# Performance work log

Measured on AMD Instinct MI355X. Metric: run time of the kernel, lower is better.

Reference implementation:

```python
import jax, jax.numpy as jnp
import numpy as np

T, B, IN, H, L = 300, 32, 320, 1024, 3  # seq, batch, input, hidden, layers (bidirectional)


def _init_params(key):
    stdv = 1.0 / np.sqrt(H)
    ks = jax.random.split(key, 8)
    u = lambda k, shp: jax.random.uniform(k, shp, jnp.float32, -stdv, stdv)
    # layer 0 (input IN), 2 directions
    w_ih0 = u(ks[0], (2, 4 * H, IN))
    w_hh0 = u(ks[1], (2, 4 * H, H))
    b_ih0 = u(ks[2], (2, 4 * H))
    b_hh0 = u(ks[3], (2, 4 * H))
    # layers 1..L-1 (input 2H), 2 directions
    w_ihL = u(ks[4], (L - 1, 2, 4 * H, 2 * H))
    w_hhL = u(ks[5], (L - 1, 2, 4 * H, H))
    b_ihL = u(ks[6], (L - 1, 2, 4 * H))
    b_hhL = u(ks[7], (L - 1, 2, 4 * H))
    # forget_gate_bias = 1.0 applied to bias_ih[H:2H], bias_hh[H:2H] = 0
    fgb = 1.0
    b_ih0 = b_ih0.at[:, H:2 * H].set(fgb)
    b_hh0 = b_hh0.at[:, H:2 * H].set(0.0)
    b_ihL = b_ihL.at[:, :, H:2 * H].set(fgb)
    b_hhL = b_hhL.at[:, :, H:2 * H].set(0.0)
    return dict(w_ih0=w_ih0, w_hh0=w_hh0, b_ih0=b_ih0, b_hh0=b_hh0,
                w_ihL=w_ihL, w_hhL=w_hhL, b_ihL=b_ihL, b_hhL=b_hhL)


def setup_inputs() -> dict:
    key = jax.random.key(0)
    k1, k2 = jax.random.split(key)
    inp = {
        "x": jax.random.normal(k1, (T, B, IN), jnp.float32),
        "h0": jnp.zeros((L * 2, B, H), jnp.float32),
        "c0": jnp.zeros((L * 2, B, H), jnp.float32),
    }
    inp.update(_init_params(k2))
    return inp


def _hard_sigmoid(z):
    return jnp.clip(0.2 * z + 0.5, 0.0, 1.0)


def _lstm_dir(x_seq, w_ih, w_hh, b_ih, b_hh, h0, c0, reverse):
    # x_seq: [T, B, D_in]; returns ys [T,B,H], (h,c) [B,H]
    xs = jnp.flip(x_seq, 0) if reverse else x_seq
    gx = jnp.einsum('tbi,gi->tbg', xs, w_ih) + b_ih + b_hh  # [T,B,4H]

    def step(carry, gxt):
        h, c = carry
        gates = gxt + h @ w_hh.T
        i, f, g, o = jnp.split(gates, 4, axis=-1)
        i = _hard_sigmoid(i)
        f = _hard_sigmoid(f)
        g = jnp.clip(g, -1.0, 1.0)  # hardtanh
        o = _hard_sigmoid(o)
        c = f * c + i * g
        h = o * jnp.clip(c, -1.0, 1.0)
        return (h, c), h

    (h, c), ys = jax.lax.scan(step, (h0, c0), gx)
    if reverse:
        ys = jnp.flip(ys, 0)
    return ys, h, c


def _stacked_forward(x, h0, c0, w_ih0, w_hh0, b_ih0, b_hh0, w_ihL, w_hhL, b_ihL, b_hhL):
    # Faithful to StackedLSTM: hn = hx[0].view(L,2,B,H); cn = hn (source bug: cell
    # init comes from h0, c0 ignored). h0/c0 are zeros so this is also correct math.
    hn = h0.reshape(L, 2, B, H)
    cn = hn
    out = x
    hs, cs = [], []
    for l in range(L):
        if l == 0:
            wih, whh, bih, bhh = w_ih0, w_hh0, b_ih0, b_hh0
        else:
            wih, whh, bih, bhh = w_ihL[l - 1], w_hhL[l - 1], b_ihL[l - 1], b_hhL[l - 1]
        yf, hf, cf = _lstm_dir(out, wih[0], whh[0], bih[0], bhh[0], hn[l, 0], cn[l, 0], False)
        yb, hb, cb = _lstm_dir(out, wih[1], whh[1], bih[1], bhh[1], hn[l, 1], cn[l, 1], True)
        out = jnp.concatenate([yf, yb], axis=-1)  # [T,B,2H]
        hs += [hf, hb]
        cs += [cf, cb]
    hn_out = jnp.stack(hs)  # [L*2, B, H]
    cn_out = jnp.stack(cs)
    return out, hn_out, cn_out


def reference(x, h0, c0, w_ih0, w_hh0, b_ih0, b_hh0, w_ihL, w_hhL, b_ihL, b_hhL):
    return _stacked_forward(x, h0, c0, w_ih0, w_hh0, b_ih0, b_hh0,
                            w_ihL, w_hhL, b_ihL, b_hhL)
```

## Files before the change

### kernel.cpp

```cpp
#include <hip/hip_runtime.h>

typedef __bf16 bf16;
typedef __attribute__((ext_vector_type(8))) __bf16 bf16x8;
typedef __attribute__((ext_vector_type(4))) float f32x4;

#define GLOBAL_AS __attribute__((address_space(1)))
#define LDS_AS __attribute__((address_space(3)))

__device__ __forceinline__ void gload_lds16(const void* g, void* l) {
  __builtin_amdgcn_global_load_lds((const GLOBAL_AS void*)g, (LDS_AS void*)l, 16, 0, 0);
}
__device__ __forceinline__ void gload_lds16_cc(const void* g, void* l) {
  __builtin_amdgcn_global_load_lds((const GLOBAL_AS void*)g, (LDS_AS void*)l, 16, 0, 0x11);
}

__device__ __forceinline__ f32x4 mfma16(bf16x8 a, bf16x8 b, f32x4 c) {
  return __builtin_amdgcn_mfma_f32_16x16x32_bf16(a, b, c, 0, 0, 0);
}

#define GBAR() asm volatile("s_barrier" ::: "memory")

#define T_SEQ 300
#define NBATCH 32
#define DIN 320
#define NH 1024
#define NG 4096
#define MROWS 9600
#define OUT_Y 19660800
#define HN_SZ 196608
#define FPAD 32

__global__ __launch_bounds__(256) void k_cvt(const float* __restrict__ src,
                                             bf16* __restrict__ dst, int n8) {
  int stride = gridDim.x * blockDim.x;
  for (int i = blockIdx.x * blockDim.x + threadIdx.x; i < n8; i += stride) {
    const float* s = src + (size_t)i * 8;
    f32x4 a = *(const f32x4*)s;
    f32x4 b = *(const f32x4*)(s + 4);
    bf16x8 o;
#pragma unroll
    for (int j = 0; j < 4; ++j) { o[j] = (bf16)a[j]; o[j + 4] = (bf16)b[j]; }
    *(bf16x8*)(dst + (size_t)i * 8) = o;
  }
}

__global__ __launch_bounds__(256) void k_bsum(const float* __restrict__ bih0,
                                              const float* __restrict__ bhh0,
                                              const float* __restrict__ bihL,
                                              const float* __restrict__ bhhL,
                                              float* __restrict__ bsum) {
  int i = blockIdx.x * 256 + threadIdx.x;
  if (i < 2 * NG) bsum[i] = bih0[i] + bhh0[i];
  else            bsum[i] = bihL[i - 2 * NG] + bhhL[i - 2 * NG];
}

__global__ __launch_bounds__(256) void k_gemm_gx(const bf16* __restrict__ A,
                                                 const bf16* __restrict__ Bw,
                                                 const float* __restrict__ bias,
                                                 bf16* __restrict__ gxout, int K) {
  __shared__ bf16 As[128 * 32];
  __shared__ bf16 Bs[128 * 32];
  const int t = threadIdx.x;
  const int m0 = blockIdx.y * 128, n0 = blockIdx.x * 128;
  const int lane = t & 63, wid = t >> 6;
  const int wr = wid >> 1, wc = wid & 1;
  const int fr = lane & 15, fq = lane >> 4;
  f32x4 acc[4][4] = {};
  for (int k0 = 0; k0 < K; k0 += 32) {
#pragma unroll
    for (int r = 0; r < 2; ++r) {
      int idx = r * 256 + t;
      int row = idx >> 2, kk = (idx & 3) * 8;
      gload_lds16(A + (size_t)(m0 + row) * K + k0 + kk, As + (size_t)idx * 8);
      gload_lds16(Bw + (size_t)(n0 + row) * K + k0 + kk, Bs + (size_t)idx * 8);
    }
    asm volatile("s_waitcnt vmcnt(0)" ::: "memory");
    __syncthreads();
    bf16x8 af[4], bf_[4];
#pragma unroll
    for (int i2 = 0; i2 < 4; ++i2) {
      af[i2]  = *(const bf16x8*)(As + (wr * 64 + i2 * 16 + fr) * 32 + fq * 8);
      bf_[i2] = *(const bf16x8*)(Bs + (wc * 64 + i2 * 16 + fr) * 32 + fq * 8);
    }
#pragma unroll
    for (int mi = 0; mi < 4; ++mi)
#pragma unroll
      for (int ni = 0; ni < 4; ++ni)
        acc[mi][ni] = mfma16(af[mi], bf_[ni], acc[mi][ni]);
    __syncthreads();
  }
#pragma unroll
  for (int ni = 0; ni < 4; ++ni) {
    int col = n0 + wc * 64 + ni * 16 + fr;
    float bv = bias[col];
    int dir = col >> 12, grow = col & (NG - 1);
    int gg = grow >> 10, uu = grow & 1023;
    bf16* base = gxout + ((size_t)dir * 300 * 4 + gg) * 32768 + uu;
#pragma unroll
    for (int mi = 0; mi < 4; ++mi) {
#pragma unroll
      for (int j = 0; j < 4; ++j) {
        int row = m0 + wr * 64 + mi * 16 + fq * 4 + j;
        int tt = row >> 5, b = row & 31;
        base[(size_t)tt * 131072 + b * 1024] = (bf16)(acc[mi][ni][j] + bv);
      }
    }
  }
}

__global__ __launch_bounds__(256) void k_init(const float* __restrict__ h0,
                                              bf16* __restrict__ hbuf,
                                              int* __restrict__ flags, int layer) {
  int i = blockIdx.x * 256 + threadIdx.x;
  hbuf[i] = (bf16)h0[(size_t)layer * 65536 + i];
  if (blockIdx.x == 0) {
    for (int j = threadIdx.x; j < 64 * FPAD; j += 256) flags[j] = 0;
  }
}

__global__ __launch_bounds__(512, 1) void k_rec(
    const bf16* __restrict__ whh,
    const bf16* __restrict__ gxT,
    const float* __restrict__ h0,
    bf16* __restrict__ hbuf,
    int* __restrict__ flags,
    bf16* __restrict__ yout,
    float* __restrict__ dout,
    int layer,
    const bf16* __restrict__ gB,
    const float* __restrict__ gbias,
    int ngemm) {
  __shared__ char smem_[131072];
  float* EX = (float*)smem_;
  char* GXL = smem_ + 67584;

  const int tid = threadIdx.x;
  const int bid = blockIdx.x;

  if (bid >= 64) {
    const int gid = bid - 64;
    if (gid >= ngemm) return;
    const int lane = tid & 63, wid = tid >> 6;
    const int wm = wid >> 1, wn = wid & 1;
    const int fr = lane & 15, fq = lane >> 4;
    const int srow = tid >> 2;
    const int scol = (tid & 3) * 8;
    const int l16 = tid * 16;
#pragma unroll 1
    for (int i = 0; i < 7; ++i) {
      const int lin = i * 192 + gid;
      if (lin >= 1216) break;
      const int n0 = (lin & 31) << 8;
      const int mrank = lin >> 5;
      const int m = (mrank & 1) ? (19 + (mrank >> 1)) : (18 - (mrank >> 1));
      const int m0 = m << 8;
      int ra = 8 * m + 7; if (ra > 299) ra = 299;
      const int rb = 299 - 8 * m;
      const int thr = (ra > rb ? ra : rb) + 2;
      if (tid < 64) {
        while (__hip_atomic_load(&flags[tid * FPAD], __ATOMIC_RELAXED,
                                 __HIP_MEMORY_SCOPE_AGENT) < thr)
          __builtin_amdgcn_s_sleep(200);
      }
      __syncthreads();
      __builtin_amdgcn_fence(__ATOMIC_ACQUIRE, "agent");

      const bf16* ArowL = yout + (size_t)(m0 + srow) * 2048 + scol;
      const bf16* ArowH = yout + (size_t)(m0 + 128 + srow) * 2048 + scol;
      const bf16* BrowL = gB + (size_t)(n0 + srow) * 2048 + scol;
      const bf16* BrowH = gB + (size_t)(n0 + 128 + srow) * 2048 + scol;

      auto stage = [&](int ks) {
        char* buf = smem_ + (ks & 3) * 32768;
        gload_lds16(ArowL + ks * 32, buf + l16);
        gload_lds16(ArowH + ks * 32, buf + 8192 + l16);
        gload_lds16(BrowL + ks * 32, buf + 16384 + l16);
        gload_lds16(BrowH + ks * 32, buf + 24576 + l16);
      };

      f32x4 acc[4][8] = {};
      auto compute = [&](int k) {
        const bf16* As = (const bf16*)(smem_ + (k & 3) * 32768);
        const bf16* Bs = As + 8192;
        bf16x8 af[4], bfv[8];
#pragma unroll
        for (int i2 = 0; i2 < 4; ++i2)
          af[i2] = *(const bf16x8*)(As + (wm * 64 + i2 * 16 + fr) * 32 + fq * 8);
#pragma unroll
        for (int i2 = 0; i2 < 8; ++i2)
          bfv[i2] = *(const bf16x8*)(Bs + (wn * 128 + i2 * 16 + fr) * 32 + fq * 8);
#pragma unroll
        for (int mi = 0; mi < 4; ++mi)
#pragma unroll
          for (int ni = 0; ni < 8; ++ni)
            acc[mi][ni] = mfma16(af[mi], bfv[ni], acc[mi][ni]);
      };

      stage(0); stage(1); stage(2); stage(3);

#pragma unroll 1
      for (int k = 0; k < 60; ++k) {
        asm volatile("s_waitcnt vmcnt(12)" ::: "memory");
        GBAR();
        __builtin_amdgcn_sched_barrier(0);
        compute(k);
        __builtin_amdgcn_sched_barrier(0);
        GBAR();
        stage(k + 4);
      }
#define GTAIL(K, WAITS)                                          \
      asm volatile("s_waitcnt vmcnt(" WAITS ")" ::: "memory");   \
      GBAR();                                                    \
      __builtin_amdgcn_sched_barrier(0);                         \
      compute(K);                                                \
      __builtin_amdgcn_sched_barrier(0);                         \
      GBAR();
      GTAIL(60, "12") GTAIL(61, "8") GTAIL(62, "4") GTAIL(63, "0")
#undef GTAIL

#pragma unroll
      for (int ni = 0; ni < 8; ++ni) {
        int col = n0 + wn * 128 + ni * 16 + fr;
        float bv = gbias[col];
        int dirv = col >> 12, grow = col & (NG - 1);
        int gg = grow >> 10, uu = grow & 1023;
        bf16* base = (bf16*)gxT + ((size_t)dirv * 1200 + gg) * 32768 + uu;
#pragma unroll
        for (int mi = 0; mi < 4; ++mi) {
#pragma unroll
          for (int j = 0; j < 4; ++j) {
            int row = m0 + wm * 64 + mi * 16 + fq * 4 + j;
            if (row < MROWS) {
              int tt = row >> 5, b = row & 31;
              base[(size_t)tt * 131072 + b * 1024] = (bf16)(acc[mi][ni][j] + bv);
            }
          }
        }
      }
    }
    return;
  }

  const int dir = bid >> 5;
  const int rank = bid & 31;
  const int u0 = rank << 5;
  const int w = tid >> 6, lane = tid & 63;
  const int fr = lane & 15, fq = lane >> 4;
  const int kh = w >> 1, rh = w & 1;

  f32x4 wf[32];
#pragma unroll
  for (int rg = 0; rg < 4; ++rg) {
    int rowb = rh * 64 + rg * 16 + fr;
    const bf16* Wp = whh + ((size_t)dir * 4096 + (rowb >> 5) * 1024 + u0 + (rowb & 31)) * 1024
                     + kh * 256 + fq * 8;
#pragma unroll
    for (int it = 0; it < 8; ++it) wf[rg * 8 + it] = *(const f32x4*)(Wp + it * 32);
  }
#pragma unroll
  for (int i = 0; i < 32; ++i) asm volatile("" : "+v"(wf[i]));

  const int b_pt = tid >> 4;
  const int ul_pt = (tid & 15) << 1;
  const int ug_pt = u0 + ul_pt;
  const size_t soff = ((size_t)layer * 2 + dir) * 32768 + (size_t)b_pt * 1024 + ug_pt;
  float c0 = h0[soff], c1 = h0[soff + 1];
  float hl0 = 0.f, hl1 = 0.f;

  const int gg = tid >> 7, sub = tid & 127;
  const size_t gx_base0 = ((size_t)dir * 1200 + gg) * 32768
                          + (size_t)(sub >> 2) * 1024 + u0 + (sub & 3) * 8;

  int srcoff[8];
#pragma unroll
  for (int r = 0; r < 8; ++r) {
    int d = r * 8192 + tid * 16;
    int row = d >> 11, colb = d & 2047;
    srcoff[r] = row * 2048 + (colb ^ ((row & 7) << 4));
  }
  const int swz = (fr & 7) << 4;

  {
    const int ts0 = dir ? (T_SEQ - 1) : 0;
    gload_lds16(gxT + gx_base0 + (size_t)ts0 * 131072, GXL + tid * 16);
  }

#pragma unroll 1
  for (int t = 0; t < T_SEQ; ++t) {
    const int tseq = dir ? (T_SEQ - 1 - t) : t;

    if (tid < 32) {
      while (__hip_atomic_load(&flags[(dir * 32 + tid) * FPAD], __ATOMIC_RELAXED,
                               __HIP_MEMORY_SCOPE_AGENT) < t)
        __builtin_amdgcn_s_sleep(1);
    }
    __syncthreads();

    const char* hsrc = (const char*)hbuf + (((size_t)(t & 1) * 2 + dir) << 16);
#pragma unroll
    for (int r = 0; r < 8; ++r)
      gload_lds16_cc(hsrc + srcoff[r], smem_ + r * 8192 + tid * 16);
    asm volatile("s_waitcnt vmcnt(0)" ::: "memory");
    __syncthreads();

    f32x4 acc[4][2] = {};
    const char* hb0 = smem_ + fr * 2048;
#pragma unroll
    for (int it = 0; it < 8; ++it) {
      int col = kh * 512 + it * 64 + fq * 16;
      bf16x8 ha0 = *(const bf16x8*)(hb0 + (col ^ swz));
      bf16x8 ha1 = *(const bf16x8*)(hb0 + 32768 + (col ^ swz));
#pragma unroll
      for (int rg = 0; rg < 4; ++rg) {
        bf16x8 wv = __builtin_bit_cast(bf16x8, wf[rg * 8 + it]);
        acc[rg][0] = mfma16(ha0, wv, acc[rg][0]);
        acc[rg][1] = mfma16(ha1, wv, acc[rg][1]);
      }
    }
    __syncthreads();

#pragma unroll
    for (int rg = 0; rg < 4; ++rg) {
      int rowb = rh * 64 + rg * 16 + fr;
      float* exr = EX + (size_t)(kh * 128 + rowb) * 33;
#pragma unroll
      for (int j = 0; j < 4; ++j) {
        exr[fq * 4 + j]      = acc[rg][0][j];
        exr[16 + fq * 4 + j] = acc[rg][1][j];
      }
    }
    __syncthreads();

    const bf16* gxb = (const bf16*)(GXL + (t & 1) * 8192);
    float hv[2]; float cc[2] = {c0, c1};
#pragma unroll
    for (int q = 0; q < 2; ++q) {
      int ul = ul_pt + q;
      float gt[4];
#pragma unroll
      for (int g2 = 0; g2 < 4; ++g2) {
        int rowb = g2 * 32 + ul;
        float s = EX[(size_t)(0 * 128 + rowb) * 33 + b_pt]
                + EX[(size_t)(1 * 128 + rowb) * 33 + b_pt]
                + EX[(size_t)(2 * 128 + rowb) * 33 + b_pt]
                + EX[(size_t)(3 * 128 + rowb) * 33 + b_pt];
        gt[g2] = s + (float)gxb[(g2 * 32 + b_pt) * 32 + ul];
      }
      float iv = fminf(fmaxf(__builtin_fmaf(0.2f, gt[0], 0.5f), 0.f), 1.f);
      float fv = fminf(fmaxf(__builtin_fmaf(0.2f, gt[1], 0.5f), 0.f), 1.f);
      float gv = fminf(fmaxf(gt[2], -1.f), 1.f);
      float ov = fminf(fmaxf(__builtin_fmaf(0.2f, gt[3], 0.5f), 0.f), 1.f);
      float c = fv * cc[q] + iv * gv;
      cc[q] = c;
      hv[q] = ov * fminf(fmaxf(c, -1.f), 1.f);
    }
    c0 = cc[0]; c1 = cc[1]; hl0 = hv[0]; hl1 = hv[1];

    unsigned hp;
    { union { bf16 h[2]; unsigned u; } pk; pk.h[0] = (bf16)hv[0]; pk.h[1] = (bf16)hv[1]; hp = pk.u; }
    volatile unsigned* hdst =
        (volatile unsigned*)((char*)hbuf + (((size_t)((t + 1) & 1) * 2 + dir) << 16))
        + (((size_t)b_pt * 1024 + ug_pt) >> 1);
    *hdst = hp;
    asm volatile("s_waitcnt vmcnt(0)" ::: "memory");
    __syncthreads();
    if (tid == 0)
      __hip_atomic_store(&flags[bid * FPAD], t + 1, __ATOMIC_RELAXED, __HIP_MEMORY_SCOPE_AGENT);

    if (yout) {
      volatile unsigned* yd =
          (volatile unsigned*)((char*)yout
              + (((size_t)tseq * 32 + b_pt) * 2048 + dir * 1024 + ug_pt) * 2);
      *yd = hp;
    } else {
      float* yd = dout + ((size_t)tseq * 32 + b_pt) * 2048 + dir * 1024 + ug_pt;
      yd[0] = hv[0]; yd[1] = hv[1];
    }
    if (t + 1 < T_SEQ) {
      const int tn = dir ? (T_SEQ - 2 - t) : (t + 1);
      gload_lds16(gxT + gx_base0 + (size_t)tn * 131072,
                  GXL + ((t + 1) & 1) * 8192 + tid * 16);
    }
  }

  dout[OUT_Y + soff] = hl0;
  dout[OUT_Y + soff + 1] = hl1;
  dout[OUT_Y + HN_SZ + soff] = c0;
  dout[OUT_Y + HN_SZ + soff + 1] = c1;
  asm volatile("s_waitcnt vmcnt(0)" ::: "memory");
  __syncthreads();
  if (tid == 0)
    __hip_atomic_store(&flags[bid * FPAD], 302, __ATOMIC_RELAXED, __HIP_MEMORY_SCOPE_AGENT);
}

extern "C" void kernel_launch(void* const* d_in, const int* in_sizes, int n_in,
                              void* d_out, int out_size, void* d_ws, size_t ws_size,
                              hipStream_t stream) {
  const float* x     = (const float*)d_in[0];
  const float* h0    = (const float*)d_in[1];
  const float* w_ih0 = (const float*)d_in[3];
  const float* w_hh0 = (const float*)d_in[4];
  const float* b_ih0 = (const float*)d_in[5];
  const float* b_hh0 = (const float*)d_in[6];
  const float* w_ihL = (const float*)d_in[7];
  const float* w_hhL = (const float*)d_in[8];
  const float* b_ihL = (const float*)d_in[9];
  const float* b_hhL = (const float*)d_in[10];
  float* dout = (float*)d_out;
  char* ws = (char*)d_ws;

  const size_t OFF_XB   = 0;
  const size_t OFF_WIH0 = 6144000;
  const size_t OFF_WIHL = 11386880;
  const size_t OFF_WHH  = 78495744;
  const size_t OFF_BSUM = 128827392;
  const size_t OFF_GX   = 128925696;
  const size_t OFF_Y0   = 286212096;
  const size_t OFF_Y1   = 325533696;
  const size_t OFF_HBF  = 364855296;
  const size_t OFF_FLG  = 365117440;

  bf16*  xb    = (bf16*)(ws + OFF_XB);
  bf16*  wih0b = (bf16*)(ws + OFF_WIH0);
  bf16*  wihLb = (bf16*)(ws + OFF_WIHL);
  bf16*  whhb  = (bf16*)(ws + OFF_WHH);
  float* bsum  = (float*)(ws + OFF_BSUM);
  bf16*  gx    = (bf16*)(ws + OFF_GX);
  bf16*  y0    = (bf16*)(ws + OFF_Y0);
  bf16*  y1    = (bf16*)(ws + OFF_Y1);
  bf16*  hbuf  = (bf16*)(ws + OFF_HBF);
  int*   flags = (int*)(ws + OFF_FLG);

  auto cvt = [&](const float* s, bf16* d, size_t n) {
    int n8 = (int)(n / 8);
    int grid = (n8 + 255) / 256; if (grid > 2048) grid = 2048;
    k_cvt<<<grid, 256, 0, stream>>>(s, d, n8);
  };

  cvt(x,     xb,    (size_t)MROWS * DIN);
  cvt(w_ih0, wih0b, (size_t)2 * NG * DIN);
  cvt(w_ihL, wihLb, (size_t)2 * 2 * NG * 2048);
  cvt(w_hh0, whhb,  (size_t)2 * NG * NH);
  cvt(w_hhL, whhb + (size_t)2 * NG * NH, (size_t)4 * NG * NH);
  k_bsum<<<96, 256, 0, stream>>>(b_ih0, b_hh0, b_ihL, b_hhL, bsum);

  k_gemm_gx<<<dim3(64, 75), 256, 0, stream>>>(xb, wih0b, bsum, gx, DIN);

  for (int l = 0; l < 3; ++l) {
    k_init<<<256, 256, 0, stream>>>(h0, hbuf, flags, l);

    const bf16* whh_l = whhb + (size_t)l * 2 * NG * NH;
    bf16* yout = (l == 0) ? y0 : (l == 1 ? y1 : nullptr);
    const int ngemm = (l < 2) ? 192 : 0;
    const bf16* gB = wihLb + (size_t)l * 2 * NG * 2048;
    const float* gbias = bsum + (size_t)(l + 1) * 2 * NG;
    k_rec<<<64 + ngemm, 512, 0, stream>>>(whh_l, gx, h0, hbuf, flags, yout, dout, l,
                                          gB, gbias, ngemm);
  }
  (void)in_sizes; (void)n_in; (void)out_size; (void)ws_size;
}
```

Measured before the change: 4.047 ms.

## Elect one XCD per direction so recurrent blocks share an L2

At kernel start each block reads its XCC_ID, and atomic elections assign one whole XCD to the forward recurrence and another to the backward recurrence. Blocks on the remaining XCDs become GEMM workers. This keeps the per-step h exchange inside a single XCD's L2, so the h loads change from system-coherent (sc0|sc1) to sc0 only and the h store becomes a plain global_store. The grid is fixed at 256 blocks, which relies on exactly 32 blocks landing on each elected XCD and on every block being co-resident; if either fails, a direction gets the wrong block count or deadlocks, and cross-XCD visibility must still hold.

```diff
diff --git a/kernel.cpp b/kernel.cpp
--- a/kernel.cpp
+++ b/kernel.cpp
@@ -10,8 +10,8 @@
 __device__ __forceinline__ void gload_lds16(const void* g, void* l) {
   __builtin_amdgcn_global_load_lds((const GLOBAL_AS void*)g, (LDS_AS void*)l, 16, 0, 0);
 }
-__device__ __forceinline__ void gload_lds16_cc(const void* g, void* l) {
-  __builtin_amdgcn_global_load_lds((const GLOBAL_AS void*)g, (LDS_AS void*)l, 16, 0, 0x11);
+__device__ __forceinline__ void gload_lds16_sc0(const void* g, void* l) {
+  __builtin_amdgcn_global_load_lds((const GLOBAL_AS void*)g, (LDS_AS void*)l, 16, 0, 0x1);
 }
 
 __device__ __forceinline__ f32x4 mfma16(bf16x8 a, bf16x8 b, f32x4 c) {
@@ -29,6 +29,11 @@
 #define OUT_Y 19660800
 #define HN_SZ 196608
 #define FPAD 32
+#define ELEC_A (64 * FPAD)
+#define ELEC_B (64 * FPAD + 8)
+#define ELEC_R0 (64 * FPAD + 16)
+#define ELEC_R1 (64 * FPAD + 24)
+#define ELEC_G (64 * FPAD + 32)
 
 __global__ __launch_bounds__(256) void k_cvt(const float* __restrict__ src,
                                              bf16* __restrict__ dst, int n8) {
@@ -115,6 +120,10 @@
   hbuf[i] = (bf16)h0[(size_t)layer * 65536 + i];
   if (blockIdx.x == 0) {
     for (int j = threadIdx.x; j < 64 * FPAD; j += 256) flags[j] = 0;
+    if (threadIdx.x == 0) {
+      flags[ELEC_A] = -1; flags[ELEC_B] = -1;
+      flags[ELEC_R0] = 0; flags[ELEC_R1] = 0; flags[ELEC_G] = 0;
+    }
   }
 }
 
@@ -133,12 +142,47 @@
   __shared__ char smem_[131072];
   float* EX = (float*)smem_;
   char* GXL = smem_ + 67584;
+  __shared__ int role2[2];
 
   const int tid = threadIdx.x;
-  const int bid = blockIdx.x;
-
-  if (bid >= 64) {
-    const int gid = bid - 64;
+
+  if (tid == 0) {
+    int xcd;
+    asm volatile("s_getreg_b32 %0, hwreg(HW_REG_XCC_ID)" : "=s"(xcd));
+    xcd &= 0xf;
+    int expct = -1;
+    __hip_atomic_compare_exchange_strong(&flags[ELEC_A], &expct, xcd,
+        __ATOMIC_ACQ_REL, __ATOMIC_RELAXED, __HIP_MEMORY_SCOPE_AGENT);
+    int A;
+    while ((A = __hip_atomic_load(&flags[ELEC_A], __ATOMIC_RELAXED,
+                                  __HIP_MEMORY_SCOPE_AGENT)) == -1) {}
+    int dir_ = -1;
+    if (xcd == A) {
+      dir_ = 0;
+    } else {
+      expct = -1;
+      __hip_atomic_compare_exchange_strong(&flags[ELEC_B], &expct, xcd,
+          __ATOMIC_ACQ_REL, __ATOMIC_RELAXED, __HIP_MEMORY_SCOPE_AGENT);
+      int B;
+      while ((B = __hip_atomic_load(&flags[ELEC_B], __ATOMIC_RELAXED,
+                                    __HIP_MEMORY_SCOPE_AGENT)) == -1) {}
+      if (xcd == B) dir_ = 1;
+    }
+    int rk;
+    if (dir_ >= 0)
+      rk = __hip_atomic_fetch_add(&flags[dir_ ? ELEC_R1 : ELEC_R0], 1,
+                                  __ATOMIC_RELAXED, __HIP_MEMORY_SCOPE_AGENT);
+    else
+      rk = __hip_atomic_fetch_add(&flags[ELEC_G], 1,
+                                  __ATOMIC_RELAXED, __HIP_MEMORY_SCOPE_AGENT);
+    role2[0] = dir_; role2[1] = rk;
+  }
+  __syncthreads();
+  const int dirx = role2[0];
+  const int rankx = role2[1];
+
+  if (dirx < 0) {
+    const int gid = rankx;
     if (gid >= ngemm) return;
     const int lane = tid & 63, wid = tid >> 6;
     const int wm = wid >> 1, wn = wid & 1;
@@ -241,12 +285,13 @@
     return;
   }
 
-  const int dir = bid >> 5;
-  const int rank = bid & 31;
+  const int dir = dirx;
+  const int rank = rankx;
   const int u0 = rank << 5;
   const int w = tid >> 6, lane = tid & 63;
   const int fr = lane & 15, fq = lane >> 4;
   const int kh = w >> 1, rh = w & 1;
+  const int fidx = (dir * 32 + rank) * FPAD;
 
   f32x4 wf[32];
 #pragma unroll
@@ -299,7 +344,7 @@
     const char* hsrc = (const char*)hbuf + (((size_t)(t & 1) * 2 + dir) << 16);
 #pragma unroll
     for (int r = 0; r < 8; ++r)
-      gload_lds16_cc(hsrc + srcoff[r], smem_ + r * 8192 + tid * 16);
+      gload_lds16_sc0(hsrc + srcoff[r], smem_ + r * 8192 + tid * 16);
     asm volatile("s_waitcnt vmcnt(0)" ::: "memory");
     __syncthreads();
 
@@ -358,14 +403,15 @@
 
     unsigned hp;
     { union { bf16 h[2]; unsigned u; } pk; pk.h[0] = (bf16)hv[0]; pk.h[1] = (bf16)hv[1]; hp = pk.u; }
-    volatile unsigned* hdst =
-        (volatile unsigned*)((char*)hbuf + (((size_t)((t + 1) & 1) * 2 + dir) << 16))
-        + (((size_t)b_pt * 1024 + ug_pt) >> 1);
-    *hdst = hp;
+    {
+      unsigned* hdst = (unsigned*)((char*)hbuf + (((size_t)((t + 1) & 1) * 2 + dir) << 16))
+                       + (((size_t)b_pt * 1024 + ug_pt) >> 1);
+      asm volatile("global_store_dword %0, %1, off" :: "v"(hdst), "v"(hp) : "memory");
+    }
     asm volatile("s_waitcnt vmcnt(0)" ::: "memory");
     __syncthreads();
     if (tid == 0)
-      __hip_atomic_store(&flags[bid * FPAD], t + 1, __ATOMIC_RELAXED, __HIP_MEMORY_SCOPE_AGENT);
+      __hip_atomic_store(&flags[fidx], t + 1, __ATOMIC_RELAXED, __HIP_MEMORY_SCOPE_AGENT);
 
     if (yout) {
       volatile unsigned* yd =
@@ -390,7 +436,7 @@
   asm volatile("s_waitcnt vmcnt(0)" ::: "memory");
   __syncthreads();
   if (tid == 0)
-    __hip_atomic_store(&flags[bid * FPAD], 302, __ATOMIC_RELAXED, __HIP_MEMORY_SCOPE_AGENT);
+    __hip_atomic_store(&flags[fidx], 302, __ATOMIC_RELAXED, __HIP_MEMORY_SCOPE_AGENT);
 }
 
 extern "C" void kernel_launch(void* const* d_in, const int* in_sizes, int n_in,
@@ -454,8 +500,8 @@
     const int ngemm = (l < 2) ? 192 : 0;
     const bf16* gB = wihLb + (size_t)l * 2 * NG * 2048;
     const float* gbias = bsum + (size_t)(l + 1) * 2 * NG;
-    k_rec<<<64 + ngemm, 512, 0, stream>>>(whh_l, gx, h0, hbuf, flags, yout, dout, l,
-                                          gB, gbias, ngemm);
+    k_rec<<<256, 512, 0, stream>>>(whh_l, gx, h0, hbuf, flags, yout, dout, l,
+                                   gB, gbias, ngemm);
   }
   (void)in_sizes; (void)n_in; (void)out_size; (void)ws_size;
 }
```

After: 3.894 ms. -3.8%, faster.
